# Kernel tuning notes

Measured on AMD Instinct MI355X. Metric: run time of the kernel, lower is better.

The kernel has to match this reference:

```python
import jax, jax.numpy as jnp
import numpy as np

D_MODEL = 256
EXPAND = 2
MAX_STEPS = 6
DILATIONS = (1, 2, 4)
EPS = 1e-6


def setup_inputs() -> dict:
    key = jax.random.key(0)
    ks = jax.random.split(key, 12)
    B, C, H, W = 8, D_MODEL, 64, 64
    d, dh = D_MODEL, D_MODEL * EXPAND
    init_logit = float(np.log(0.1 / (0.25 - 0.1 + 1e-08)))
    s = 1.0 / np.sqrt(d)
    return {
        "u": jax.random.normal(ks[0], (B, C, H, W), jnp.float32),
        "forcing": jax.random.normal(ks[1], (B, C, H, W), jnp.float32),
        "diff_logits": jnp.full((3, d), init_logit, jnp.float32),
        "w1": jax.random.uniform(ks[2], (d, dh), jnp.float32, -s, s),
        "b1": jax.random.uniform(ks[3], (dh,), jnp.float32, -s, s),
        "w2": jax.random.uniform(ks[4], (dh, d), jnp.float32, -1.0 / np.sqrt(dh), 1.0 / np.sqrt(dh)),
        "b2": jax.random.uniform(ks[5], (d,), jnp.float32, -1.0 / np.sqrt(dh), 1.0 / np.sqrt(dh)),
        "wf": jax.random.uniform(ks[6], (d, d), jnp.float32, -s, s),
        "bf": jax.random.uniform(ks[7], (d,), jnp.float32, -s, s),
        "wi": jax.random.uniform(ks[8], (d, d), jnp.float32, -s, s),
        "bi": jax.random.uniform(ks[9], (d,), jnp.float32, -s, s),
        "wc": jax.random.uniform(ks[10], (d, d), jnp.float32, -s, s),
        "bc": jax.random.uniform(ks[11], (d,), jnp.float32, -s, s),
        "norm_scale": jnp.ones((d,), jnp.float32),
        "log_dt": jnp.asarray(np.log(0.1), jnp.float32),
        "alpha_mem": jnp.asarray(0.1, jnp.float32),
        "alpha_force": jnp.asarray(0.1, jnp.float32),
    }


def _laplacian(u, diff_logits):
    # multi-dilation 5-point reflect-padded stencil, per-channel coeffs
    out = jnp.zeros_like(u)
    for i, d in enumerate(DILATIONS):
        coeff = 0.25 * jax.nn.sigmoid(diff_logits[i])  # (C,)
        p = jnp.pad(u, ((0, 0), (0, 0), (d, d), (d, d)), mode="reflect")
        lap = (p[:, :, d:-d, 2 * d:] + p[:, :, d:-d, :-2 * d]
               + p[:, :, 2 * d:, d:-d] + p[:, :, :-2 * d, d:-d] - 4.0 * u)
        out = out + coeff[None, :, None, None] * lap
    return out


def reference(u, forcing, diff_logits, w1, b1, w2, b2, wf, bf, wi, bi, wc, bc,
              norm_scale, log_dt, alpha_mem, alpha_force):
    B, C, H, W = u.shape
    dt = jnp.clip(jnp.exp(log_dt), 0.01, 0.3)
    h = jnp.zeros((B, C), u.dtype)
    inv_sqrt_c = 1.0 / float(np.sqrt(C))
    for t in range(MAX_STEPS):
        diff = _laplacian(u, diff_logits)
        # per-cell reaction MLP on channel axis (exact GELU, matching torch)
        hdn = jax.nn.gelu(jnp.einsum("bchw,ce->behw", u, w1) + b1[None, :, None, None],
                          approximate=False)
        react = jnp.einsum("behw,ec->bchw", hdn, w2) + b2[None, :, None, None]
        # gated global memory on pooled features
        pooled = u.mean(axis=(2, 3))  # (B, C)
        f = jax.nn.sigmoid(pooled @ wf + bf)
        i_ = jax.nn.sigmoid(pooled @ wi + bi)
        c = jnp.tanh(pooled @ wc + bc)
        h = h * f + i_ * c
        du = diff + react + alpha_mem * h[:, :, None, None] + alpha_force * forcing
        u = u + dt * du
        if (t + 1) % 2 == 0:
            # RMSNorm over channel dim
            rms = jnp.sqrt(jnp.sum(u * u, axis=1, keepdims=True)) * inv_sqrt_c
            u = u / (rms + EPS) * norm_scale[None, :, None, None]
    return u
```

## Files before the change

### kernel.cpp

```cpp
#include <hip/hip_runtime.h>
#include <math.h>

constexpr int NB = 8, NC = 256, NE = 512, NH = 64, NW = 64, NHW = NH * NW;
constexpr int STEPS = 6;

typedef short bfrag8 __attribute__((ext_vector_type(8)));
typedef float f32x4 __attribute__((ext_vector_type(4)));

__device__ __forceinline__ float sigm_(float x) { return 1.f / (1.f + expf(-x)); }
__device__ __forceinline__ float gelu_(float x) {
    const float t2 = fmaf(0.0713548162f * x, x * x, 1.5957691216f * x);
    return x / (1.f + __expf(-t2));
}
__device__ __forceinline__ ushort f2bf(float f) {
    unsigned u = __builtin_bit_cast(unsigned, f);
    unsigned r = (u + 0x7fffu + ((u >> 16) & 1u)) >> 16;
    return (ushort)r;
}
__device__ __forceinline__ float bf2f(ushort us) {
    return __builtin_bit_cast(float, (unsigned)us << 16);
}
__device__ __forceinline__ void gload16(const void* g, void* l) {
    __builtin_amdgcn_global_load_lds((const __attribute__((address_space(1))) void*)g,
                                     (__attribute__((address_space(3))) void*)l, 16, 0, 0);
}

__global__ void wt_kernel(const float* __restrict__ w1, const float* __restrict__ w2,
                          const float* __restrict__ dlog,
                          ushort* __restrict__ w1t, ushort* __restrict__ w2t,
                          float* __restrict__ dcoef) {
    const int bid = blockIdx.x, tid = threadIdx.x;
    if (bid < NE) {
        w1t[bid * NC + tid] = f2bf(w1[(size_t)tid * NE + bid]);
    } else if (bid < NE + NC) {
        const int c = bid - NE;
        for (int e = tid; e < NE; e += 256)
            w2t[c * NE + e] = f2bf(w2[(size_t)e * NC + c]);
    } else {
#pragma unroll
        for (int i = 0; i < 3; ++i)
            dcoef[i * NC + tid] = 0.25f * sigm_(dlog[i * NC + tid]);
    }
}

__global__ void fconv_kernel(const float* __restrict__ fin, ushort* __restrict__ fout) {
    const size_t i8 = ((size_t)blockIdx.x * 256 + threadIdx.x) * 8;
    const float4 a = *reinterpret_cast<const float4*>(fin + i8);
    const float4 b = *reinterpret_cast<const float4*>(fin + i8 + 4);
    uint4 o;
    o.x = (unsigned)f2bf(a.x) | ((unsigned)f2bf(a.y) << 16);
    o.y = (unsigned)f2bf(a.z) | ((unsigned)f2bf(a.w) << 16);
    o.z = (unsigned)f2bf(b.x) | ((unsigned)f2bf(b.y) << 16);
    o.w = (unsigned)f2bf(b.z) | ((unsigned)f2bf(b.w) << 16);
    *reinterpret_cast<uint4*>(fout + i8) = o;
}

__global__ __launch_bounds__(256) void x0_kernel(const float* __restrict__ u,
                                                 ushort* __restrict__ X,
                                                 float* __restrict__ rowsums) {
    __shared__ ushort xs[64][264];
    const int tid = threadIdx.x;
    const int b = blockIdx.x >> 6, y = blockIdx.x & 63;
    const float* up = u + (size_t)b * NC * NHW + y * NW;
#pragma unroll
    for (int cc = 0; cc < 4; ++cc)
#pragma unroll
        for (int i = 0; i < 16; ++i) {
            const int idx = i * 256 + tid;
            const int c = idx >> 6, x = idx & 63;
            xs[x][cc * 64 + c] = f2bf(up[(size_t)(cc * 64 + c) * NHW + x]);
        }
    __syncthreads();
    ushort* Xp = X + ((size_t)b * NHW + y * NW) * NC;
    const int wv = tid >> 6, lane = tid & 63;
#pragma unroll
    for (int r = 0; r < 16; ++r) {
        const int row = wv * 16 + r;
        *reinterpret_cast<uint2*>(Xp + (size_t)row * NC + lane * 4) =
            *reinterpret_cast<const uint2*>(&xs[row][lane * 4]);
    }
    const float* rp = up + (size_t)tid * NHW;
    float s = 0.f;
#pragma unroll
    for (int x = 0; x < 64; ++x) s += rp[x];
    rowsums[((size_t)b * 64 + y) * NC + tid] = s;
}

__global__ __launch_bounds__(768) void gates_kernel(
    const float* __restrict__ rowsums,
    const float* __restrict__ wf, const float* __restrict__ bfv,
    const float* __restrict__ wi, const float* __restrict__ biv,
    const float* __restrict__ wc, const float* __restrict__ bcv,
    float* __restrict__ h, const int first) {
    const int b = blockIdx.x;
    const int tid = threadIdx.x;
    const int g = tid >> 8, c = tid & 255;
    __shared__ float sp[256];
    __shared__ float psum[3][256];
    __shared__ float gf[256], gi[256];
    const int y0 = (g == 0) ? 0 : (g == 1) ? 21 : 42;
    const int y1 = (g == 0) ? 21 : (g == 1) ? 42 : 64;
    const float* rs = rowsums + (size_t)b * 64 * NC + c;
    float s = 0.f;
    for (int y = y0; y < y1; ++y) s += rs[y * NC];
    psum[g][c] = s;
    __syncthreads();
    if (g == 0) sp[c] = (psum[0][c] + psum[1][c] + psum[2][c]) * (1.f / 4096.f);
    __syncthreads();
    const float* W  = (g == 0) ? wf  : (g == 1) ? wi  : wc;
    const float* Bv = (g == 0) ? bfv : (g == 1) ? biv : bcv;
    float aA = 0.f, aB = 0.f, aC = 0.f, aD = 0.f;
#pragma unroll 4
    for (int k = 0; k < 256; k += 4) {
        aA = fmaf(sp[k],     W[(size_t)(k)     * NC + c], aA);
        aB = fmaf(sp[k + 1], W[(size_t)(k + 1) * NC + c], aB);
        aC = fmaf(sp[k + 2], W[(size_t)(k + 2) * NC + c], aC);
        aD = fmaf(sp[k + 3], W[(size_t)(k + 3) * NC + c], aD);
    }
    const float a = ((aA + aB) + (aC + aD)) + Bv[c];
    if (g == 0) gf[c] = sigm_(a);
    else if (g == 1) gi[c] = sigm_(a);
    __syncthreads();
    if (g == 2) {
        const float cc = tanhf(a);
        const float hold = first ? 0.f : h[b * NC + c];
        h[b * NC + c] = hold * gf[c] + gi[c] * cc;
    }
}

__global__ __launch_bounds__(512, 4) void step_kernel(
    const ushort* __restrict__ Xg, const ushort* __restrict__ w1t,
    const ushort* __restrict__ w2t, const float* __restrict__ b1,
    const float* __restrict__ b2, const float* __restrict__ uin,
    const ushort* __restrict__ forc, const float* __restrict__ dcoef,
    const float* __restrict__ hbuf, const float* __restrict__ nsc,
    const float* __restrict__ p_logdt, const float* __restrict__ p_am,
    const float* __restrict__ p_af, const int do_norm,
    float* __restrict__ uout, ushort* __restrict__ Xout,
    float* __restrict__ rowsums) {
    __shared__ __align__(16) char pool[75776];
    ushort* Xs  = (ushort*)pool;
    ushort* WAu = (ushort*)(pool + 32768);
    ushort* WBu = (ushort*)(pool + 49152);
    ushort* Hsu = (ushort*)(pool + 65536);

    const int tid = threadIdx.x;
    const int wv = tid >> 6, lane = tid & 63;
    const int r16 = lane & 15, kg = lane >> 4;
    const int work = (blockIdx.x & 7) * 64 + (blockIdx.x >> 3);
    const int b = work >> 6, y = work & 63;
    const int m0 = work * 64;

#pragma unroll
    for (int i = 0; i < 4; ++i) {
        const int idx = i * 512 + tid, row = idx >> 5, s = idx & 31;
        gload16(Xg + (size_t)(m0 + row) * NC + ((s ^ (row & 7)) << 3), Xs + idx * 8);
    }
#pragma unroll
    for (int i = 0; i < 2; ++i) {
        const int idx = i * 512 + tid, row = idx >> 5, s = idx & 31;
        gload16(w1t + (size_t)row * NC + ((s ^ (row & 7)) << 3), WAu + idx * 8);
    }

    f32x4 acc2[2][4];
#pragma unroll
    for (int ct = 0; ct < 2; ++ct)
#pragma unroll
        for (int p = 0; p < 4; ++p) acc2[ct][p] = (f32x4){0.f, 0.f, 0.f, 0.f};

    const int eh = wv >> 2, pq = wv & 3;
    __syncthreads();

    for (int ec = 0; ec < 16; ++ec) {
#pragma unroll
        for (int i = 0; i < 2; ++i) {
            const int idx = i * 512 + tid, row = idx >> 2, s = idx & 3;
            const int sc = (s ^ ((row >> 1) & 3)) << 3;
            gload16(w2t + (size_t)row * NE + ec * 32 + sc, WBu + idx * 8);
        }
        f32x4 acc1 = (f32x4){0.f, 0.f, 0.f, 0.f};
        const int rA = eh * 16 + r16, rB = pq * 16 + r16;
#pragma unroll
        for (int kk = 0; kk < 8; ++kk) {
            const int g = kk * 4 + kg;
            const bfrag8 a = *(const bfrag8*)(WAu + rA * 256 + ((g ^ (rA & 7)) << 3));
            const bfrag8 bb = *(const bfrag8*)(Xs + rB * 256 + ((g ^ (rB & 7)) << 3));
            acc1 = __builtin_amdgcn_mfma_f32_16x16x32_bf16(a, bb, acc1, 0, 0, 0);
        }
        ushort* Hc = Hsu + (ec & 1) * 2560;
        {
            const int el = eh * 16 + kg * 4;
            const float4 b1v = *(const float4*)(b1 + ec * 32 + el);
            ushort4 hv;
            hv.x = f2bf(gelu_(acc1[0] + b1v.x));
            hv.y = f2bf(gelu_(acc1[1] + b1v.y));
            hv.z = f2bf(gelu_(acc1[2] + b1v.z));
            hv.w = f2bf(gelu_(acc1[3] + b1v.w));
            *(ushort4*)(Hc + (pq * 16 + r16) * 40 + el) = hv;
        }
        __syncthreads();
        if (ec < 15) {
#pragma unroll
            for (int i = 0; i < 2; ++i) {
                const int idx = i * 512 + tid, row = idx >> 5, s = idx & 31;
                gload16(w1t + (size_t)((ec + 1) * 32 + row) * NC + ((s ^ (row & 7)) << 3),
                        WAu + idx * 8);
            }
        }
#pragma unroll
        for (int ct = 0; ct < 2; ++ct) {
            const int rowA = wv * 32 + ct * 16 + r16;
            const bfrag8 a2 = *(const bfrag8*)(WBu + rowA * 32 + ((kg ^ ((rowA >> 1) & 3)) << 3));
#pragma unroll
            for (int p = 0; p < 4; ++p) {
                const bfrag8 bf2 = *(const bfrag8*)(Hc + (p * 16 + r16) * 40 + kg * 8);
                acc2[ct][p] = __builtin_amdgcn_mfma_f32_16x16x32_bf16(a2, bf2, acc2[ct][p], 0, 0, 0);
            }
        }
        __syncthreads();
    }

    float* trh = (float*)pool;
    float* su  = (float*)(pool + 34816);
    const int eg2 = tid >> 4, pg = tid & 15, x0p = pg * 4;
    const float dt = fminf(fmaxf(expf(p_logdt[0]), 0.01f), 0.3f);
    const float am = p_am[0], afc = p_af[0];
    const float* ub = uin + (size_t)b * NC * NHW;
    const ushort* frow = forc + (size_t)b * NC * NHW + (size_t)y * NW;

    float unew[2][4][4];

#pragma unroll
    for (int h2 = 0; h2 < 2; ++h2) {
        __syncthreads();
        if ((wv >> 2) == h2) {
#pragma unroll
            for (int ct = 0; ct < 2; ++ct)
#pragma unroll
                for (int p = 0; p < 4; ++p)
#pragma unroll
                    for (int j = 0; j < 4; ++j)
                        trh[((wv & 3) * 32 + ct * 16 + kg * 4 + j) * 68 + p * 16 + r16] =
                            acc2[ct][p][j];
        }
#pragma unroll
        for (int i = 0; i < 4; ++i) {
            const int idx = i * 512 + tid;
            const int r = idx >> 4, q = (idx & 15) * 4;
            *(float4*)&su[r * 68 + q] =
                *(const float4*)(ub + (size_t)(h2 * 128 + r) * NHW + (size_t)y * NW + q);
        }
        __syncthreads();
#pragma unroll
        for (int jc = 0; jc < 4; ++jc) {
            const int crel = eg2 * 4 + jc;
            const int c = h2 * 128 + crel;
            const float co0 = dcoef[c];
            const float co1 = dcoef[NC + c];
            const float co2 = dcoef[2 * NC + c];
            const float hterm = am * hbuf[b * NC + c];
            const float b2v = b2[c];
            const float* up = ub + (size_t)c * NHW;

            float ym[6][4];
            const int dy[6] = {-1, 1, -2, 2, -4, 4};
#pragma unroll
            for (int n = 0; n < 6; ++n) {
                int ry = y + dy[n];
                ry = ry < 0 ? -ry : (ry > 63 ? 126 - ry : ry);
                const float4 t = *reinterpret_cast<const float4*>(up + (size_t)ry * NW + x0p);
                ym[n][0] = t.x; ym[n][1] = t.y; ym[n][2] = t.z; ym[n][3] = t.w;
            }
            const uint2 fr = *reinterpret_cast<const uint2*>(frow + (size_t)c * NHW + x0p);
            float fv[4];
            fv[0] = bf2f((ushort)(fr.x & 0xffff));
            fv[1] = bf2f((ushort)(fr.x >> 16));
            fv[2] = bf2f((ushort)(fr.y & 0xffff));
            fv[3] = bf2f((ushort)(fr.y >> 16));
            const f32x4 rv = *reinterpret_cast<const f32x4*>(&trh[crel * 68 + x0p]);
#pragma unroll
            for (int ip = 0; ip < 4; ++ip) {
                const int x = x0p + ip;
                const float uc = su[crel * 68 + x];
                int xm, xp2;
                float dsum = 0.f, lap;
                xm = x - 1; xm = xm < 0 ? -xm : xm;
                xp2 = x + 1; xp2 = xp2 > 63 ? 126 - xp2 : xp2;
                lap = su[crel * 68 + xm] + su[crel * 68 + xp2] + ym[0][ip] + ym[1][ip] - 4.f * uc;
                dsum = fmaf(co0, lap, dsum);
                xm = x - 2; xm = xm < 0 ? -xm : xm;
                xp2 = x + 2; xp2 = xp2 > 63 ? 126 - xp2 : xp2;
                lap = su[crel * 68 + xm] + su[crel * 68 + xp2] + ym[2][ip] + ym[3][ip] - 4.f * uc;
                dsum = fmaf(co1, lap, dsum);
                xm = x - 4; xm = xm < 0 ? -xm : xm;
                xp2 = x + 4; xp2 = xp2 > 63 ? 126 - xp2 : xp2;
                lap = su[crel * 68 + xm] + su[crel * 68 + xp2] + ym[4][ip] + ym[5][ip] - 4.f * uc;
                dsum = fmaf(co2, lap, dsum);

                const float du_ = dsum + rv[ip] + b2v + hterm + afc * fv[ip];
                unew[h2][jc][ip] = uc + dt * du_;
            }
        }
    }
    __syncthreads();

    float* redc   = (float*)(pool + 34816);
    float* inv64p = (float*)(pool + 43520);
    if (do_norm) {
        float ps[4] = {0.f, 0.f, 0.f, 0.f};
#pragma unroll
        for (int h2 = 0; h2 < 2; ++h2)
#pragma unroll
            for (int jc = 0; jc < 4; ++jc)
#pragma unroll
                for (int ip = 0; ip < 4; ++ip)
                    ps[ip] = fmaf(unew[h2][jc][ip], unew[h2][jc][ip], ps[ip]);
        *reinterpret_cast<f32x4*>(&redc[eg2 * 68 + x0p]) = (f32x4){ps[0], ps[1], ps[2], ps[3]};
        __syncthreads();
        if (tid < 64) {
            float s = 0.f;
#pragma unroll
            for (int g = 0; g < 32; ++g) s += redc[g * 68 + tid];
            inv64p[tid] = 1.f / (sqrtf(s) * 0.0625f + 1e-6f);
        }
    }
    __syncthreads();

    ushort* xs = (ushort*)pool;
    float* sums = (float*)(pool + 52224);
    float persum[2][4];
    float* uob = uout + (size_t)b * NC * NHW + (size_t)y * NW;
#pragma unroll
    for (int h2 = 0; h2 < 2; ++h2) {
        float vsc[4][4];
#pragma unroll
        for (int jc = 0; jc < 4; ++jc) {
            const int c = h2 * 128 + eg2 * 4 + jc;
            const float ns = do_norm ? nsc[c] : 1.f;
#pragma unroll
            for (int ip = 0; ip < 4; ++ip) {
                float v = unew[h2][jc][ip];
                if (do_norm) v *= inv64p[x0p + ip] * ns;
                vsc[jc][ip] = v;
            }
            persum[h2][jc] = vsc[jc][0] + vsc[jc][1] + vsc[jc][2] + vsc[jc][3];
            float4 o; o.x = vsc[jc][0]; o.y = vsc[jc][1]; o.z = vsc[jc][2]; o.w = vsc[jc][3];
            *reinterpret_cast<float4*>(uob + (size_t)c * NHW + x0p) = o;
        }
#pragma unroll
        for (int ip = 0; ip < 4; ++ip) {
            ushort4 xv;
            xv.x = f2bf(vsc[0][ip]);
            xv.y = f2bf(vsc[1][ip]);
            xv.z = f2bf(vsc[2][ip]);
            xv.w = f2bf(vsc[3][ip]);
            *(ushort4*)(xs + (x0p + ip) * 270 + h2 * 128 + eg2 * 4) = xv;
        }
    }
#pragma unroll
    for (int h2 = 0; h2 < 2; ++h2)
#pragma unroll
        for (int jc = 0; jc < 4; ++jc)
            sums[(h2 * 128 + eg2 * 4 + jc) * 17 + pg] = persum[h2][jc];
    __syncthreads();
    ushort* Xp = Xout + (size_t)m0 * NC;
#pragma unroll
    for (int r = 0; r < 8; ++r) {
        const int row = wv * 8 + r;
        *reinterpret_cast<uint2*>(Xp + (size_t)row * NC + lane * 4) =
            *reinterpret_cast<const uint2*>(&xs[row * 270 + lane * 4]);
    }
    if (tid < 256) {
        float s = 0.f;
#pragma unroll
        for (int g = 0; g < 16; ++g) s += sums[tid * 17 + g];
        rowsums[((size_t)b * 64 + y) * NC + tid] = s;
    }
}

extern "C" void kernel_launch(void* const* d_in, const int* in_sizes, int n_in,
                              void* d_out, int out_size, void* d_ws, size_t ws_size,
                              hipStream_t stream) {
    (void)in_sizes; (void)n_in; (void)out_size; (void)ws_size;
    const float* u0      = (const float*)d_in[0];
    const float* forcing = (const float*)d_in[1];
    const float* dlog    = (const float*)d_in[2];
    const float* w1      = (const float*)d_in[3];
    const float* b1      = (const float*)d_in[4];
    const float* w2      = (const float*)d_in[5];
    const float* b2      = (const float*)d_in[6];
    const float* wf      = (const float*)d_in[7];
    const float* bfv     = (const float*)d_in[8];
    const float* wi      = (const float*)d_in[9];
    const float* biv     = (const float*)d_in[10];
    const float* wc      = (const float*)d_in[11];
    const float* bcv     = (const float*)d_in[12];
    const float* nsc     = (const float*)d_in[13];
    const float* p_logdt = (const float*)d_in[14];
    const float* p_am    = (const float*)d_in[15];
    const float* p_af    = (const float*)d_in[16];

    float* uout = (float*)d_out;

    char* w = (char*)d_ws;
    float*  uA     = (float*)w;   w += (size_t)NB * NC * NHW * 4;
    ushort* X      = (ushort*)w;  w += (size_t)NB * NHW * NC * 2;
    ushort* forc   = (ushort*)w;  w += (size_t)NB * NC * NHW * 2;
    ushort* w1t    = (ushort*)w;  w += (size_t)NE * NC * 2;
    ushort* w2t    = (ushort*)w;  w += (size_t)NC * NE * 2;
    float* rowsums = (float*)w;   w += (size_t)NB * NH * NC * 4;
    float* hbuf    = (float*)w;   w += (size_t)NB * NC * 4;
    float* dcoef   = (float*)w;   w += (size_t)3 * NC * 4;

    wt_kernel<<<769, 256, 0, stream>>>(w1, w2, dlog, w1t, w2t, dcoef);
    fconv_kernel<<<4096, 256, 0, stream>>>(forcing, forc);
    x0_kernel<<<NB * NH, 256, 0, stream>>>(u0, X, rowsums);

    const float* src = u0;
    for (int t = 0; t < STEPS; ++t) {
        float* dst = (t & 1) ? uout : uA;
        gates_kernel<<<NB, 768, 0, stream>>>(rowsums, wf, bfv, wi, biv, wc, bcv, hbuf, t == 0);
        step_kernel<<<NB * NH, 512, 0, stream>>>(X, w1t, w2t, b1, b2, src, forc, dcoef,
                                                 hbuf, nsc, p_logdt, p_am, p_af,
                                                 ((t + 1) % 2) == 0, dst, X, rowsums);
        src = dst;
    }
}
```

Before: 576.5 us.

## Build bf16 channel-last tile in-kernel from fp32 u instead of separate X buffer

The step kernel no longer reads a precomputed bf16 pixel-major X buffer, and no longer writes one for the next step. It loads the fp32 u row directly, converts it to bf16 and transposes it into swizzled LDS, removing a global write plus read of X per step. The initial x0 kernel becomes a plain rowsum kernel. The gate weights are also pre-converted to bf16 so the small gates kernel reads half the bytes. The cost is more fp32 global reads and conversion work at the start of each step block, and slightly lower precision in the gates.

```diff
diff --git a/kernel.cpp b/kernel.cpp
--- a/kernel.cpp
+++ b/kernel.cpp
@@ -27,8 +27,10 @@
 
 __global__ void wt_kernel(const float* __restrict__ w1, const float* __restrict__ w2,
                           const float* __restrict__ dlog,
+                          const float* __restrict__ wf, const float* __restrict__ wi,
+                          const float* __restrict__ wc,
                           ushort* __restrict__ w1t, ushort* __restrict__ w2t,
-                          float* __restrict__ dcoef) {
+                          float* __restrict__ dcoef, ushort* __restrict__ wgb) {
     const int bid = blockIdx.x, tid = threadIdx.x;
     if (bid < NE) {
         w1t[bid * NC + tid] = f2bf(w1[(size_t)tid * NE + bid]);
@@ -36,10 +38,15 @@
         const int c = bid - NE;
         for (int e = tid; e < NE; e += 256)
             w2t[c * NE + e] = f2bf(w2[(size_t)e * NC + c]);
-    } else {
+    } else if (bid == NE + NC) {
 #pragma unroll
         for (int i = 0; i < 3; ++i)
             dcoef[i * NC + tid] = 0.25f * sigm_(dlog[i * NC + tid]);
+    } else {
+        const int k = bid - (NE + NC + 1);
+        wgb[(0 * NC + k) * NC + tid] = f2bf(wf[(size_t)k * NC + tid]);
+        wgb[(1 * NC + k) * NC + tid] = f2bf(wi[(size_t)k * NC + tid]);
+        wgb[(2 * NC + k) * NC + tid] = f2bf(wc[(size_t)k * NC + tid]);
     }
 }
 
@@ -55,42 +62,24 @@
     *reinterpret_cast<uint4*>(fout + i8) = o;
 }
 
-__global__ __launch_bounds__(256) void x0_kernel(const float* __restrict__ u,
-                                                 ushort* __restrict__ X,
-                                                 float* __restrict__ rowsums) {
-    __shared__ ushort xs[64][264];
-    const int tid = threadIdx.x;
+__global__ __launch_bounds__(256) void rs0_kernel(const float* __restrict__ u,
+                                                  float* __restrict__ rowsums) {
     const int b = blockIdx.x >> 6, y = blockIdx.x & 63;
-    const float* up = u + (size_t)b * NC * NHW + y * NW;
-#pragma unroll
-    for (int cc = 0; cc < 4; ++cc)
-#pragma unroll
-        for (int i = 0; i < 16; ++i) {
-            const int idx = i * 256 + tid;
-            const int c = idx >> 6, x = idx & 63;
-            xs[x][cc * 64 + c] = f2bf(up[(size_t)(cc * 64 + c) * NHW + x]);
-        }
-    __syncthreads();
-    ushort* Xp = X + ((size_t)b * NHW + y * NW) * NC;
-    const int wv = tid >> 6, lane = tid & 63;
-#pragma unroll
-    for (int r = 0; r < 16; ++r) {
-        const int row = wv * 16 + r;
-        *reinterpret_cast<uint2*>(Xp + (size_t)row * NC + lane * 4) =
-            *reinterpret_cast<const uint2*>(&xs[row][lane * 4]);
-    }
-    const float* rp = up + (size_t)tid * NHW;
+    const int c = threadIdx.x;
+    const float* rp = u + ((size_t)b * NC + c) * NHW + (size_t)y * NW;
     float s = 0.f;
 #pragma unroll
-    for (int x = 0; x < 64; ++x) s += rp[x];
-    rowsums[((size_t)b * 64 + y) * NC + tid] = s;
+    for (int i = 0; i < 16; ++i) {
+        const float4 v = *reinterpret_cast<const float4*>(rp + i * 4);
+        s += (v.x + v.y) + (v.z + v.w);
+    }
+    rowsums[((size_t)b * 64 + y) * NC + c] = s;
 }
 
 __global__ __launch_bounds__(768) void gates_kernel(
-    const float* __restrict__ rowsums,
-    const float* __restrict__ wf, const float* __restrict__ bfv,
-    const float* __restrict__ wi, const float* __restrict__ biv,
-    const float* __restrict__ wc, const float* __restrict__ bcv,
+    const float* __restrict__ rowsums, const ushort* __restrict__ wgb,
+    const float* __restrict__ bfv, const float* __restrict__ biv,
+    const float* __restrict__ bcv,
     float* __restrict__ h, const int first) {
     const int b = blockIdx.x;
     const int tid = threadIdx.x;
@@ -107,15 +96,15 @@
     __syncthreads();
     if (g == 0) sp[c] = (psum[0][c] + psum[1][c] + psum[2][c]) * (1.f / 4096.f);
     __syncthreads();
-    const float* W  = (g == 0) ? wf  : (g == 1) ? wi  : wc;
+    const ushort* W16 = wgb + (size_t)g * NC * NC;
     const float* Bv = (g == 0) ? bfv : (g == 1) ? biv : bcv;
     float aA = 0.f, aB = 0.f, aC = 0.f, aD = 0.f;
 #pragma unroll 4
     for (int k = 0; k < 256; k += 4) {
-        aA = fmaf(sp[k],     W[(size_t)(k)     * NC + c], aA);
-        aB = fmaf(sp[k + 1], W[(size_t)(k + 1) * NC + c], aB);
-        aC = fmaf(sp[k + 2], W[(size_t)(k + 2) * NC + c], aC);
-        aD = fmaf(sp[k + 3], W[(size_t)(k + 3) * NC + c], aD);
+        aA = fmaf(sp[k],     bf2f(W16[(k)     * NC + c]), aA);
+        aB = fmaf(sp[k + 1], bf2f(W16[(k + 1) * NC + c]), aB);
+        aC = fmaf(sp[k + 2], bf2f(W16[(k + 2) * NC + c]), aC);
+        aD = fmaf(sp[k + 3], bf2f(W16[(k + 3) * NC + c]), aD);
     }
     const float a = ((aA + aB) + (aC + aD)) + Bv[c];
     if (g == 0) gf[c] = sigm_(a);
@@ -129,15 +118,13 @@
 }
 
 __global__ __launch_bounds__(512, 4) void step_kernel(
-    const ushort* __restrict__ Xg, const ushort* __restrict__ w1t,
-    const ushort* __restrict__ w2t, const float* __restrict__ b1,
-    const float* __restrict__ b2, const float* __restrict__ uin,
-    const ushort* __restrict__ forc, const float* __restrict__ dcoef,
-    const float* __restrict__ hbuf, const float* __restrict__ nsc,
-    const float* __restrict__ p_logdt, const float* __restrict__ p_am,
-    const float* __restrict__ p_af, const int do_norm,
-    float* __restrict__ uout, ushort* __restrict__ Xout,
-    float* __restrict__ rowsums) {
+    const ushort* __restrict__ w1t, const ushort* __restrict__ w2t,
+    const float* __restrict__ b1, const float* __restrict__ b2,
+    const float* __restrict__ uin, const ushort* __restrict__ forc,
+    const float* __restrict__ dcoef, const float* __restrict__ hbuf,
+    const float* __restrict__ nsc, const float* __restrict__ p_logdt,
+    const float* __restrict__ p_am, const float* __restrict__ p_af,
+    const int do_norm, float* __restrict__ uout, float* __restrict__ rowsums) {
     __shared__ __align__(16) char pool[75776];
     ushort* Xs  = (ushort*)pool;
     ushort* WAu = (ushort*)(pool + 32768);
@@ -149,17 +136,39 @@
     const int r16 = lane & 15, kg = lane >> 4;
     const int work = (blockIdx.x & 7) * 64 + (blockIdx.x >> 3);
     const int b = work >> 6, y = work & 63;
-    const int m0 = work * 64;
-
-#pragma unroll
-    for (int i = 0; i < 4; ++i) {
-        const int idx = i * 512 + tid, row = idx >> 5, s = idx & 31;
-        gload16(Xg + (size_t)(m0 + row) * NC + ((s ^ (row & 7)) << 3), Xs + idx * 8);
-    }
+
+    const float* ub = uin + (size_t)b * NC * NHW;
+    const float* uyb = ub + (size_t)y * NW;
+
 #pragma unroll
     for (int i = 0; i < 2; ++i) {
         const int idx = i * 512 + tid, row = idx >> 5, s = idx & 31;
         gload16(w1t + (size_t)row * NC + ((s ^ (row & 7)) << 3), WAu + idx * 8);
+    }
+#pragma unroll
+    for (int tt = 0; tt < 2; ++tt) {
+        const int id = tt * 512 + tid;
+        const int pg_ = id & 15, cg_ = id >> 4;
+        const int px0 = pg_ * 4, c0 = cg_ * 4;
+        const float4 r0 = *(const float4*)(uyb + (size_t)(c0 + 0) * NHW + px0);
+        const float4 r1 = *(const float4*)(uyb + (size_t)(c0 + 1) * NHW + px0);
+        const float4 r2 = *(const float4*)(uyb + (size_t)(c0 + 2) * NHW + px0);
+        const float4 r3 = *(const float4*)(uyb + (size_t)(c0 + 3) * NHW + px0);
+        const int slot = c0 >> 3, sub = c0 & 7;
+        const float a0[4] = {r0.x, r0.y, r0.z, r0.w};
+        const float a1[4] = {r1.x, r1.y, r1.z, r1.w};
+        const float a2[4] = {r2.x, r2.y, r2.z, r2.w};
+        const float a3[4] = {r3.x, r3.y, r3.z, r3.w};
+#pragma unroll
+        for (int i2 = 0; i2 < 4; ++i2) {
+            const int px = px0 + i2;
+            ushort4 xv;
+            xv.x = f2bf(a0[i2]);
+            xv.y = f2bf(a1[i2]);
+            xv.z = f2bf(a2[i2]);
+            xv.w = f2bf(a3[i2]);
+            *(ushort4*)(Xs + px * 256 + ((slot ^ (px & 7)) << 3) + sub) = xv;
+        }
     }
 
     f32x4 acc2[2][4];
@@ -225,7 +234,6 @@
     const int eg2 = tid >> 4, pg = tid & 15, x0p = pg * 4;
     const float dt = fminf(fmaxf(expf(p_logdt[0]), 0.01f), 0.3f);
     const float am = p_am[0], afc = p_af[0];
-    const float* ub = uin + (size_t)b * NC * NHW;
     const ushort* frow = forc + (size_t)b * NC * NHW + (size_t)y * NW;
 
     float unew[2][4][4];
@@ -326,50 +334,29 @@
     }
     __syncthreads();
 
-    ushort* xs = (ushort*)pool;
     float* sums = (float*)(pool + 52224);
     float persum[2][4];
     float* uob = uout + (size_t)b * NC * NHW + (size_t)y * NW;
 #pragma unroll
     for (int h2 = 0; h2 < 2; ++h2) {
-        float vsc[4][4];
 #pragma unroll
         for (int jc = 0; jc < 4; ++jc) {
             const int c = h2 * 128 + eg2 * 4 + jc;
             const float ns = do_norm ? nsc[c] : 1.f;
+            float vv[4];
 #pragma unroll
             for (int ip = 0; ip < 4; ++ip) {
                 float v = unew[h2][jc][ip];
                 if (do_norm) v *= inv64p[x0p + ip] * ns;
-                vsc[jc][ip] = v;
+                vv[ip] = v;
             }
-            persum[h2][jc] = vsc[jc][0] + vsc[jc][1] + vsc[jc][2] + vsc[jc][3];
-            float4 o; o.x = vsc[jc][0]; o.y = vsc[jc][1]; o.z = vsc[jc][2]; o.w = vsc[jc][3];
+            persum[h2][jc] = (vv[0] + vv[1]) + (vv[2] + vv[3]);
+            float4 o; o.x = vv[0]; o.y = vv[1]; o.z = vv[2]; o.w = vv[3];
             *reinterpret_cast<float4*>(uob + (size_t)c * NHW + x0p) = o;
-        }
-#pragma unroll
-        for (int ip = 0; ip < 4; ++ip) {
-            ushort4 xv;
-            xv.x = f2bf(vsc[0][ip]);
-            xv.y = f2bf(vsc[1][ip]);
-            xv.z = f2bf(vsc[2][ip]);
-            xv.w = f2bf(vsc[3][ip]);
-            *(ushort4*)(xs + (x0p + ip) * 270 + h2 * 128 + eg2 * 4) = xv;
-        }
-    }
-#pragma unroll
-    for (int h2 = 0; h2 < 2; ++h2)
-#pragma unroll
-        for (int jc = 0; jc < 4; ++jc)
-            sums[(h2 * 128 + eg2 * 4 + jc) * 17 + pg] = persum[h2][jc];
-    __syncthreads();
-    ushort* Xp = Xout + (size_t)m0 * NC;
-#pragma unroll
-    for (int r = 0; r < 8; ++r) {
-        const int row = wv * 8 + r;
-        *reinterpret_cast<uint2*>(Xp + (size_t)row * NC + lane * 4) =
-            *reinterpret_cast<const uint2*>(&xs[row * 270 + lane * 4]);
-    }
+            sums[c * 17 + pg] = persum[h2][jc];
+        }
+    }
+    __syncthreads();
     if (tid < 256) {
         float s = 0.f;
 #pragma unroll
@@ -404,25 +391,26 @@
 
     char* w = (char*)d_ws;
     float*  uA     = (float*)w;   w += (size_t)NB * NC * NHW * 4;
-    ushort* X      = (ushort*)w;  w += (size_t)NB * NHW * NC * 2;
     ushort* forc   = (ushort*)w;  w += (size_t)NB * NC * NHW * 2;
     ushort* w1t    = (ushort*)w;  w += (size_t)NE * NC * 2;
     ushort* w2t    = (ushort*)w;  w += (size_t)NC * NE * 2;
+    ushort* wgb    = (ushort*)w;  w += (size_t)3 * NC * NC * 2;
     float* rowsums = (float*)w;   w += (size_t)NB * NH * NC * 4;
     float* hbuf    = (float*)w;   w += (size_t)NB * NC * 4;
     float* dcoef   = (float*)w;   w += (size_t)3 * NC * 4;
 
-    wt_kernel<<<769, 256, 0, stream>>>(w1, w2, dlog, w1t, w2t, dcoef);
+    wt_kernel<<<NE + NC + 1 + NC, 256, 0, stream>>>(w1, w2, dlog, wf, wi, wc,
+                                                    w1t, w2t, dcoef, wgb);
     fconv_kernel<<<4096, 256, 0, stream>>>(forcing, forc);
-    x0_kernel<<<NB * NH, 256, 0, stream>>>(u0, X, rowsums);
+    rs0_kernel<<<NB * NH, 256, 0, stream>>>(u0, rowsums);
 
     const float* src = u0;
     for (int t = 0; t < STEPS; ++t) {
         float* dst = (t & 1) ? uout : uA;
-        gates_kernel<<<NB, 768, 0, stream>>>(rowsums, wf, bfv, wi, biv, wc, bcv, hbuf, t == 0);
-        step_kernel<<<NB * NH, 512, 0, stream>>>(X, w1t, w2t, b1, b2, src, forc, dcoef,
+        gates_kernel<<<NB, 768, 0, stream>>>(rowsums, wgb, bfv, biv, bcv, hbuf, t == 0);
+        step_kernel<<<NB * NH, 512, 0, stream>>>(w1t, w2t, b1, b2, src, forc, dcoef,
                                                  hbuf, nsc, p_logdt, p_am, p_af,
-                                                 ((t + 1) % 2) == 0, dst, X, rowsums);
+                                                 ((t + 1) % 2) == 0, dst, rowsums);
         src = dst;
     }
 }
```

Result: no change. 565.9 us (median of 2 runs) (-1.8%).
